# Optimization experiments

Hardware: AMD Instinct MI355X
Metric: run time of the kernel (lower is better)

## Reference

```python
import jax, jax.numpy as jnp
import numpy as np

LAYERS = 30
LAYERS_PER_STACK = 10  # layers // stacks
UPSAMPLE_SCALES = (10, 8)


def _c1x1(w, x):
    # 1x1 conv: w [O,C], x [B,C,T] -> [B,O,T]
    return jnp.einsum('oc,bct->bot', w, x)


def setup_inputs() -> dict:
    key = jax.random.key(0)
    ks = jax.random.split(key, 16)
    B, T, F = 4, 32000, 400
    s = 0.1  # weight scale to keep gates unsaturated
    inp = {
        'x': jax.random.normal(ks[0], (B, 256, T), jnp.float32),
        'c': jax.random.normal(ks[1], (B, 80, F), jnp.float32),
        'first_w': jax.random.normal(ks[2], (64, 256), jnp.float32) * s,
        'first_b': jnp.zeros((64,), jnp.float32),
        'conv_w': jax.random.normal(ks[3], (LAYERS, 128, 64, 2), jnp.float32) * s,
        'conv_b': jnp.zeros((LAYERS, 128), jnp.float32),
        'cond_w': jax.random.normal(ks[4], (LAYERS, 128, 80), jnp.float32) * s,
        'out_w': jax.random.normal(ks[5], (LAYERS, 64, 64), jnp.float32) * s,
        'out_b': jnp.zeros((LAYERS, 64), jnp.float32),
        'skip_w': jax.random.normal(ks[6], (LAYERS, 64, 64), jnp.float32) * s,
        'skip_b': jnp.zeros((LAYERS, 64), jnp.float32),
        'last1_w': jax.random.normal(ks[7], (64, 64), jnp.float32) * s,
        'last1_b': jnp.zeros((64,), jnp.float32),
        'last2_w': jax.random.normal(ks[8], (256, 64), jnp.float32) * s,
        'last2_b': jnp.zeros((256,), jnp.float32),
        'conv_in_w': jax.random.normal(ks[9], (80, 80), jnp.float32) * s,
        # upsample smoothing kernels, torch init: constant 1/kernel_size
        'up_w0': jnp.full((2 * 10 + 1,), 1.0 / (2 * 10 + 1), jnp.float32),
        'up_w1': jnp.full((2 * 8 + 1,), 1.0 / (2 * 8 + 1), jnp.float32),
    }
    return inp


def _wavenet(x, c, first_w, first_b, conv_w, conv_b, cond_w, out_w, out_b,
             skip_w, skip_b, last1_w, last1_b, last2_w, last2_b, conv_in_w,
             up_w0, up_w1):
    # --- ConvInUpsampleNetwork (aux_context_window=0 -> conv_in is 1x1, no bias) ---
    c = _c1x1(conv_in_w, c)  # [B,80,F]
    C = c.shape[1]
    for scale, w in zip(UPSAMPLE_SCALES, (up_w0, up_w1)):
        c = jnp.repeat(c, scale, axis=2)  # nearest interpolate along time
        rhs = jnp.broadcast_to(w[None, None, :], (C, 1, w.shape[0]))  # depthwise avg
        c = jax.lax.conv_general_dilated(
            c, rhs, window_strides=(1,), padding=[(scale, scale)],
            feature_group_count=C, dimension_numbers=('NCH', 'OIH', 'NCH'))
    # c now [B,80,T] with T = F*80 matching x
    T = x.shape[2]

    # --- first 1x1 conv ---
    h = _c1x1(first_w, x) + first_b[None, :, None]  # [B,64,T]

    skips = jnp.zeros_like(h[:, :64, :]) * 0.0  # [B,64,T]
    skips = 0.0
    for l in range(LAYERS):
        d = 2 ** (l % LAYERS_PER_STACK)  # dilation; padding = (k-1)*d = d
        xp = jnp.pad(h, ((0, 0), (0, 0), (d, 0)))  # causal left pad
        # dilated conv, kernel_size=2: taps at t-d and t
        g = (jnp.einsum('oc,bct->bot', conv_w[l, :, :, 0], xp[:, :, :T])
             + jnp.einsum('oc,bct->bot', conv_w[l, :, :, 1], xp[:, :, d:d + T])
             + conv_b[l][None, :, None])  # [B,128,T]
        g = g + _c1x1(cond_w[l], c)  # conditioning (split(a,b)+split(ca,cb) == split(g+cc))
        a, b = jnp.split(g, 2, axis=1)
        z = jnp.tanh(a) * jax.nn.sigmoid(b)  # [B,64,T]
        skips = skips + _c1x1(skip_w[l], z) + skip_b[l][None, :, None]
        h = h + _c1x1(out_w[l], z) + out_b[l][None, :, None]

    # --- last conv layers: ReLU, 1x1, ReLU, 1x1 ---
    o = jax.nn.relu(skips)
    o = _c1x1(last1_w, o) + last1_b[None, :, None]
    o = jax.nn.relu(o)
    o = _c1x1(last2_w, o) + last2_b[None, :, None]
    return o  # [B,256,T]


def reference(x, c, first_w, first_b, conv_w, conv_b, cond_w, out_w, out_b,
              skip_w, skip_b, last1_w, last1_b, last2_w, last2_b, conv_in_w,
              up_w0, up_w1):
    return _wavenet(x, c, first_w, first_b, conv_w, conv_b, cond_w, out_w,
                    out_b, skip_w, skip_b, last1_w, last1_b, last2_w, last2_b,
                    conv_in_w, up_w0, up_w1)
```

## Files before the change

kernel.cpp:

```cpp
#include <hip/hip_runtime.h>
#include <math.h>

#define T_TOTAL 32000
#define BATCH 4
#define TT 64
#define TTL 32
#define TTF 32

typedef __bf16 bf16x8 __attribute__((ext_vector_type(8)));
typedef float f32x4 __attribute__((ext_vector_type(4)));
typedef unsigned int uint4v __attribute__((ext_vector_type(4)));
typedef unsigned int uint2v __attribute__((ext_vector_type(2)));

__device__ __forceinline__ unsigned short f2b(float f) {
    unsigned int u = __float_as_uint(f);
    u += 0x7FFFu + ((u >> 16) & 1u);
    return (unsigned short)(u >> 16);
}
__device__ __forceinline__ unsigned int f2b2(float lo, float hi) {
    return (unsigned int)f2b(lo) | ((unsigned int)f2b(hi) << 16);
}
__device__ __forceinline__ bf16x8 ld_bf8(const unsigned short* p) {
    return __builtin_bit_cast(bf16x8, *(const uint4v*)p);
}
__device__ __forceinline__ float fast_sigmoid(float x) {
    return __builtin_amdgcn_rcpf(1.0f + __expf(-x));
}
__device__ __forceinline__ float fast_tanh(float x) {
    return 1.0f - 2.0f * __builtin_amdgcn_rcpf(1.0f + __expf(2.0f * x));
}

__global__ void k_pack(const float* __restrict__ conv_w, const float* __restrict__ cond_w,
                       const float* __restrict__ skip_w, const float* __restrict__ out_w,
                       const float* __restrict__ first_w, const float* __restrict__ last1_w,
                       const float* __restrict__ last2_w,
                       unsigned short* __restrict__ wgp, unsigned short* __restrict__ wzp,
                       unsigned short* __restrict__ fwp, unsigned short* __restrict__ l1p,
                       unsigned short* __restrict__ l2p) {
    int i = blockIdx.x * blockDim.x + threadIdx.x;
    if (i < 860160) {
        int l = i / 28672, r = i % 28672;
        int o = r / 224, k = r % 224;
        float v;
        if (k < 64)       v = conv_w[(((size_t)l * 128 + o) * 64 + k) * 2 + 0];
        else if (k < 128) v = conv_w[(((size_t)l * 128 + o) * 64 + (k - 64)) * 2 + 1];
        else if (k < 208) v = cond_w[((size_t)l * 128 + o) * 80 + (k - 128)];
        else              v = 0.0f;
        wgp[i] = f2b(v);
        return;
    }
    i -= 860160;
    if (i < 245760) {
        int l = i / 8192, rr = (i % 8192) / 64, k = i % 64;
        float v = (rr < 64) ? skip_w[((size_t)l * 64 + rr) * 64 + k]
                            : out_w[((size_t)l * 64 + (rr - 64)) * 64 + k];
        wzp[i] = f2b(v);
        return;
    }
    i -= 245760;
    if (i < 16384) { fwp[i] = f2b(first_w[i]); return; }
    i -= 16384;
    if (i < 4096) { l1p[i] = f2b(last1_w[i]); return; }
    i -= 4096;
    if (i < 16384) { l2p[i] = f2b(last2_w[i]); return; }
}

__global__ void k_convin(const float* __restrict__ c, const float* __restrict__ w,
                         float* __restrict__ c1) {
    int idx = blockIdx.x * blockDim.x + threadIdx.x;
    if (idx >= BATCH * 80 * 400) return;
    int f = idx % 400;
    int o = (idx / 400) % 80;
    int b = idx / (400 * 80);
    const float* cb = c + (size_t)b * 80 * 400 + f;
    const float* wr = w + o * 80;
    float acc = 0.f;
    #pragma unroll 8
    for (int j = 0; j < 80; ++j) acc += wr[j] * cb[(size_t)j * 400];
    c1[idx] = acc;
}

__global__ void k_up0(const float* __restrict__ c1, const float* __restrict__ w,
                      float* __restrict__ c2) {
    int idx = blockIdx.x * blockDim.x + threadIdx.x;
    if (idx >= BATCH * 80 * 4000) return;
    int t = idx % 4000;
    int ch = idx / 4000;
    int u = t / 10, r = t - u * 10;
    float w0 = 0.f, w1 = 0.f, w2 = 0.f;
    #pragma unroll
    for (int j = 0; j < 21; ++j) {
        float wj = w[j];
        int a = r - 10 + j;
        if (a < 0) w0 += wj;
        else if (a < 10) w1 += wj;
        else w2 += wj;
    }
    const float* src = c1 + (size_t)ch * 400;
    float s0 = (u >= 1) ? src[u - 1] : 0.f;
    float s1 = src[u];
    float s2 = (u + 1 < 400) ? src[u + 1] : 0.f;
    c2[idx] = w0 * s0 + w1 * s1 + w2 * s2;
}

__global__ __launch_bounds__(256) void k_up1b(const float* __restrict__ c2,
                                              const float* __restrict__ w,
                                              unsigned short* __restrict__ cupb) {
    __shared__ float S[80][13];
    __shared__ float W[8][4];
    const int b = blockIdx.y, t0 = blockIdx.x * 64;
    const int tid = threadIdx.x;
    const int u0 = t0 >> 3;

    for (int i = tid; i < 800; i += 256) {
        int ch = i / 10, uu = i % 10;
        int u = u0 - 1 + uu;
        float v = 0.f;
        if (u >= 0 && u < 4000) v = c2[((size_t)b * 80 + ch) * 4000 + u];
        S[ch][uu] = v;
    }
    if (tid < 24) {
        int r = tid / 3, k = tid % 3;
        int jlo = (k == 0) ? 0 : (k == 1 ? 8 - r : 16 - r);
        int jhi = (k == 0) ? 7 - r : (k == 1 ? 15 - r : 16);
        float a = 0.f;
        for (int j = jlo; j <= jhi; ++j) a += w[j];
        W[r][k] = a;
    }
    __syncthreads();

    unsigned short* ob = cupb + ((size_t)b * T_TOTAL + t0) * 96;
    for (int i = tid; i < 64 * 96; i += 256) {
        int ch = i % 96;
        int tl = i / 96;
        float acc = 0.f;
        if (ch < 80) {
            int r = tl & 7, ub = tl >> 3;
            acc = W[r][0] * S[ch][ub] + W[r][1] * S[ch][ub + 1] + W[r][2] * S[ch][ub + 2];
        }
        ob[i] = f2b(acc);
    }
}

#define XFS 266
__global__ __launch_bounds__(256, 8) void k_first(
    const float* __restrict__ x, const unsigned short* __restrict__ fwp,
    const float* __restrict__ fb, float* __restrict__ h0) {
    __shared__ unsigned short Xf[TTF * XFS];
    const int b = blockIdx.y, t0 = blockIdx.x * TTF, tid = threadIdx.x;
    const int lane = tid & 63;
    const int wv = __builtin_amdgcn_readfirstlane(tid >> 6);
    const int l15 = lane & 15, q = lane >> 4;

    for (int i = tid; i < 2048; i += 256) {
        int ch = i >> 3;
        int t4 = (i & 7) << 2;
        const float* xr = x + ((size_t)b * 256 + ch) * T_TOTAL + t0 + t4;
        float4 u = *(const float4*)xr;
        int base = t4 * XFS + ch;
        Xf[base + 0 * XFS] = f2b(u.x);
        Xf[base + 1 * XFS] = f2b(u.y);
        Xf[base + 2 * XFS] = f2b(u.z);
        Xf[base + 3 * XFS] = f2b(u.w);
    }
    __syncthreads();

    f32x4 acc[2] = {};
    const unsigned short* wr = fwp + (size_t)(16 * wv + l15) * 256;
    #pragma unroll
    for (int ks = 0; ks < 8; ++ks) {
        bf16x8 aA = ld_bf8(wr + ks * 32 + q * 8);
        #pragma unroll
        for (int tt = 0; tt < 2; ++tt) {
            bf16x8 bb = ld_bf8(&Xf[(tt * 16 + l15) * XFS + ks * 32 + q * 8]);
            acc[tt] = __builtin_amdgcn_mfma_f32_16x16x32_bf16(aA, bb, acc[tt], 0, 0, 0);
        }
    }
    const float4 fbv = *(const float4*)&fb[16 * wv + 4 * q];
    float* hob = h0 + (size_t)b * T_TOTAL * 64;
    #pragma unroll
    for (int tt = 0; tt < 2; ++tt) {
        size_t base = (size_t)(t0 + tt * 16 + l15) * 64 + 16 * wv + 4 * q;
        float4 ho;
        ho.x = acc[tt][0] + fbv.x;
        ho.y = acc[tt][1] + fbv.y;
        ho.z = acc[tt][2] + fbv.z;
        ho.w = acc[tt][3] + fbv.w;
        *(float4*)(hob + base) = ho;
    }
}

__global__ __launch_bounds__(256, 8) void k_layer(
    const float* __restrict__ h_in, float* __restrict__ h_out,
    float* __restrict__ skips, const unsigned short* __restrict__ cupb,
    const unsigned short* __restrict__ wgp_l, const unsigned short* __restrict__ wzp_l,
    const float* __restrict__ cb_l, const float* __restrict__ ob_l,
    const float* __restrict__ sb_l, int d, int first) {
    __shared__ unsigned short Xl[TTL * 224];
    __shared__ unsigned short zs[TTL * 72];
    const int b = blockIdx.y, t0 = blockIdx.x * TTL, tid = threadIdx.x;
    const int lane = tid & 63;
    const int wv = __builtin_amdgcn_readfirstlane(tid >> 6);
    const int l15 = lane & 15, q = lane >> 4;

    const float* hb = h_in + (size_t)b * T_TOTAL * 64;
    {
        int i = tid;
        int t = i >> 3, cb8 = (i & 7) << 3;
        const float4* p1 = (const float4*)(hb + (size_t)(t0 + t) * 64 + cb8);
        float4 u0 = p1[0], u1 = p1[1];
        uint4v v1;
        v1.x = f2b2(u0.x, u0.y); v1.y = f2b2(u0.z, u0.w);
        v1.z = f2b2(u1.x, u1.y); v1.w = f2b2(u1.z, u1.w);
        *(uint4v*)&Xl[t * 224 + 64 + cb8] = v1;
        int td = t0 + t - d;
        uint4v v0 = {0u, 0u, 0u, 0u};
        if (td >= 0) {
            const float4* p0 = (const float4*)(hb + (size_t)td * 64 + cb8);
            float4 w0 = p0[0], w1 = p0[1];
            v0.x = f2b2(w0.x, w0.y); v0.y = f2b2(w0.z, w0.w);
            v0.z = f2b2(w1.x, w1.y); v0.w = f2b2(w1.z, w1.w);
        }
        *(uint4v*)&Xl[t * 224 + cb8] = v0;
    }
    const unsigned short* cbb = cupb + (size_t)b * T_TOTAL * 96;
    for (int i = tid; i < 384; i += 256) {
        int t = i / 12, j = (i % 12) << 3;
        *(uint4v*)&Xl[t * 224 + 128 + j] = *(const uint4v*)&cbb[(size_t)(t0 + t) * 96 + j];
    }
    __syncthreads();

    f32x4 accA[2] = {}, accG[2] = {};
    const unsigned short* wrow_a = wgp_l + (size_t)(16 * wv + l15) * 224;
    const unsigned short* wrow_g = wgp_l + (size_t)(64 + 16 * wv + l15) * 224;
    #pragma unroll
    for (int ks = 0; ks < 7; ++ks) {
        bf16x8 aA = ld_bf8(wrow_a + ks * 32 + q * 8);
        bf16x8 aG = ld_bf8(wrow_g + ks * 32 + q * 8);
        #pragma unroll
        for (int tt = 0; tt < 2; ++tt) {
            bf16x8 bb = ld_bf8(&Xl[(tt * 16 + l15) * 224 + ks * 32 + q * 8]);
            accA[tt] = __builtin_amdgcn_mfma_f32_16x16x32_bf16(aA, bb, accA[tt], 0, 0, 0);
            accG[tt] = __builtin_amdgcn_mfma_f32_16x16x32_bf16(aG, bb, accG[tt], 0, 0, 0);
        }
    }
    const float4 cbA = *(const float4*)&cb_l[16 * wv + 4 * q];
    const float4 cbG = *(const float4*)&cb_l[64 + 16 * wv + 4 * q];
    #pragma unroll
    for (int tt = 0; tt < 2; ++tt) {
        int t = tt * 16 + l15;
        float z0 = fast_tanh(accA[tt][0] + cbA.x) * fast_sigmoid(accG[tt][0] + cbG.x);
        float z1 = fast_tanh(accA[tt][1] + cbA.y) * fast_sigmoid(accG[tt][1] + cbG.y);
        float z2 = fast_tanh(accA[tt][2] + cbA.z) * fast_sigmoid(accG[tt][2] + cbG.z);
        float z3 = fast_tanh(accA[tt][3] + cbA.w) * fast_sigmoid(accG[tt][3] + cbG.w);
        uint2v zv;
        zv.x = f2b2(z0, z1);
        zv.y = f2b2(z2, z3);
        *(uint2v*)&zs[t * 72 + 16 * wv + 4 * q] = zv;
    }
    __syncthreads();

    f32x4 accS[2] = {}, accO[2] = {};
    const unsigned short* zrow_s = wzp_l + (size_t)(16 * wv + l15) * 64;
    const unsigned short* zrow_o = wzp_l + (size_t)(64 + 16 * wv + l15) * 64;
    #pragma unroll
    for (int ks = 0; ks < 2; ++ks) {
        bf16x8 aS = ld_bf8(zrow_s + ks * 32 + q * 8);
        bf16x8 aO = ld_bf8(zrow_o + ks * 32 + q * 8);
        #pragma unroll
        for (int tt = 0; tt < 2; ++tt) {
            bf16x8 bb = ld_bf8(&zs[(tt * 16 + l15) * 72 + ks * 32 + q * 8]);
            accS[tt] = __builtin_amdgcn_mfma_f32_16x16x32_bf16(aS, bb, accS[tt], 0, 0, 0);
            accO[tt] = __builtin_amdgcn_mfma_f32_16x16x32_bf16(aO, bb, accO[tt], 0, 0, 0);
        }
    }
    const float4 sbv = *(const float4*)&sb_l[16 * wv + 4 * q];
    const float4 obv = *(const float4*)&ob_l[16 * wv + 4 * q];
    float* hob = h_out + (size_t)b * T_TOTAL * 64;
    float* skb = skips + (size_t)b * T_TOTAL * 64;
    #pragma unroll
    for (int tt = 0; tt < 2; ++tt) {
        size_t base = (size_t)(t0 + tt * 16 + l15) * 64 + 16 * wv + 4 * q;
        float4 hi = *(const float4*)(hb + base);
        float4 ho;
        ho.x = hi.x + accO[tt][0] + obv.x;
        ho.y = hi.y + accO[tt][1] + obv.y;
        ho.z = hi.z + accO[tt][2] + obv.z;
        ho.w = hi.w + accO[tt][3] + obv.w;
        *(float4*)(hob + base) = ho;
        float4 sv;
        if (first) {
            sv.x = accS[tt][0] + sbv.x;
            sv.y = accS[tt][1] + sbv.y;
            sv.z = accS[tt][2] + sbv.z;
            sv.w = accS[tt][3] + sbv.w;
        } else {
            float4 sp = *(const float4*)(skb + base);
            sv.x = sp.x + accS[tt][0] + sbv.x;
            sv.y = sp.y + accS[tt][1] + sbv.y;
            sv.z = sp.z + accS[tt][2] + sbv.z;
            sv.w = sp.w + accS[tt][3] + sbv.w;
        }
        *(float4*)(skb + base) = sv;
    }
}

__global__ __launch_bounds__(256) void k_last(
    const float* __restrict__ skips, const unsigned short* __restrict__ l1p,
    const float* __restrict__ b1, const unsigned short* __restrict__ l2p,
    const float* __restrict__ b2, float* __restrict__ out) {
    __shared__ unsigned short sp[64 * 72];
    __shared__ unsigned short o2s[64 * 72];
    const int b = blockIdx.y, t0 = blockIdx.x * TT, tid = threadIdx.x;
    const int lane = tid & 63;
    const int wv = __builtin_amdgcn_readfirstlane(tid >> 6);
    const int l15 = lane & 15, q = lane >> 4;

    const float* skb = skips + (size_t)b * T_TOTAL * 64;
    for (int i = tid; i < 512; i += 256) {
        int t = i >> 3, cb8 = (i & 7) << 3;
        const float4* p = (const float4*)(skb + (size_t)(t0 + t) * 64 + cb8);
        float4 u0 = p[0], u1 = p[1];
        uint4v v;
        v.x = f2b2(fmaxf(u0.x, 0.f), fmaxf(u0.y, 0.f));
        v.y = f2b2(fmaxf(u0.z, 0.f), fmaxf(u0.w, 0.f));
        v.z = f2b2(fmaxf(u1.x, 0.f), fmaxf(u1.y, 0.f));
        v.w = f2b2(fmaxf(u1.z, 0.f), fmaxf(u1.w, 0.f));
        *(uint4v*)&sp[t * 72 + cb8] = v;
    }
    __syncthreads();

    f32x4 a1[4] = {};
    const unsigned short* w1r = l1p + (size_t)(16 * wv + l15) * 64;
    #pragma unroll
    for (int ks = 0; ks < 2; ++ks) {
        bf16x8 aA = ld_bf8(w1r + ks * 32 + q * 8);
        #pragma unroll
        for (int tt = 0; tt < 4; ++tt) {
            bf16x8 bb = ld_bf8(&sp[(tt * 16 + l15) * 72 + ks * 32 + q * 8]);
            a1[tt] = __builtin_amdgcn_mfma_f32_16x16x32_bf16(aA, bb, a1[tt], 0, 0, 0);
        }
    }
    const float4 b1v = *(const float4*)&b1[16 * wv + 4 * q];
    #pragma unroll
    for (int tt = 0; tt < 4; ++tt) {
        int t = tt * 16 + l15;
        float z0 = fmaxf(a1[tt][0] + b1v.x, 0.f);
        float z1 = fmaxf(a1[tt][1] + b1v.y, 0.f);
        float z2 = fmaxf(a1[tt][2] + b1v.z, 0.f);
        float z3 = fmaxf(a1[tt][3] + b1v.w, 0.f);
        uint2v zv;
        zv.x = f2b2(z0, z1);
        zv.y = f2b2(z2, z3);
        *(uint2v*)&o2s[t * 72 + 16 * wv + 4 * q] = zv;
    }
    __syncthreads();

    f32x4 a2[4][4] = {};
    #pragma unroll
    for (int ks = 0; ks < 2; ++ks) {
        bf16x8 aw[4];
        #pragma unroll
        for (int j = 0; j < 4; ++j)
            aw[j] = ld_bf8(l2p + (size_t)(64 * wv + 16 * j + l15) * 64 + ks * 32 + q * 8);
        #pragma unroll
        for (int tt = 0; tt < 4; ++tt) {
            bf16x8 bb = ld_bf8(&o2s[(tt * 16 + l15) * 72 + ks * 32 + q * 8]);
            #pragma unroll
            for (int j = 0; j < 4; ++j)
                a2[j][tt] = __builtin_amdgcn_mfma_f32_16x16x32_bf16(aw[j], bb, a2[j][tt], 0, 0, 0);
        }
    }
    float* ob = out + (size_t)b * 256 * T_TOTAL;
    #pragma unroll
    for (int j = 0; j < 4; ++j) {
        int o0 = 64 * wv + 16 * j + 4 * q;
        float4 b2v = *(const float4*)&b2[o0];
        #pragma unroll
        for (int tt = 0; tt < 4; ++tt) {
            int t = t0 + tt * 16 + l15;
            ob[(size_t)(o0 + 0) * T_TOTAL + t] = a2[j][tt][0] + b2v.x;
            ob[(size_t)(o0 + 1) * T_TOTAL + t] = a2[j][tt][1] + b2v.y;
            ob[(size_t)(o0 + 2) * T_TOTAL + t] = a2[j][tt][2] + b2v.z;
            ob[(size_t)(o0 + 3) * T_TOTAL + t] = a2[j][tt][3] + b2v.w;
        }
    }
}

extern "C" void kernel_launch(void* const* d_in, const int* in_sizes, int n_in,
                              void* d_out, int out_size, void* d_ws, size_t ws_size,
                              hipStream_t stream) {
    const float* x         = (const float*)d_in[0];
    const float* c         = (const float*)d_in[1];
    const float* first_w   = (const float*)d_in[2];
    const float* first_b   = (const float*)d_in[3];
    const float* conv_w    = (const float*)d_in[4];
    const float* conv_b    = (const float*)d_in[5];
    const float* cond_w    = (const float*)d_in[6];
    const float* out_w     = (const float*)d_in[7];
    const float* out_b     = (const float*)d_in[8];
    const float* skip_w    = (const float*)d_in[9];
    const float* skip_b    = (const float*)d_in[10];
    const float* last1_w   = (const float*)d_in[11];
    const float* last1_b   = (const float*)d_in[12];
    const float* last2_w   = (const float*)d_in[13];
    const float* last2_b   = (const float*)d_in[14];
    const float* conv_in_w = (const float*)d_in[15];
    const float* up_w0     = (const float*)d_in[16];
    const float* up_w1     = (const float*)d_in[17];

    unsigned char* base = (unsigned char*)d_ws;
    float* c1            = (float*)(base + 0);
    float* c2            = (float*)(base + 512000);
    unsigned short* cupb = (unsigned short*)(base + 5632000);
    float* hA            = (float*)(base + 30208000);
    float* hB            = (float*)(base + 62976000);
    float* skips         = (float*)(base + 95744000);
    unsigned short* wgp  = (unsigned short*)(base + 128512000);
    unsigned short* wzp  = (unsigned short*)(base + 130232320);
    unsigned short* fwp  = (unsigned short*)(base + 130723840);
    unsigned short* l1p  = (unsigned short*)(base + 130756608);
    unsigned short* l2p  = (unsigned short*)(base + 130764800);

    k_pack<<<(1142784 + 255) / 256, 256, 0, stream>>>(
        conv_w, cond_w, skip_w, out_w, first_w, last1_w, last2_w,
        wgp, wzp, fwp, l1p, l2p);
    k_convin<<<(BATCH * 80 * 400 + 255) / 256, 256, 0, stream>>>(c, conv_in_w, c1);
    k_up0<<<(BATCH * 80 * 4000 + 255) / 256, 256, 0, stream>>>(c1, up_w0, c2);
    dim3 upg(T_TOTAL / 64, BATCH);
    k_up1b<<<upg, 256, 0, stream>>>(c2, up_w1, cupb);

    dim3 gridF(T_TOTAL / TTF, BATCH);
    k_first<<<gridF, 256, 0, stream>>>(x, fwp, first_b, hA);

    dim3 gridL(T_TOTAL / TTL, BATCH);
    float* hin = hA;
    float* hout = hB;
    for (int l = 0; l < 30; ++l) {
        int d = 1 << (l % 10);
        k_layer<<<gridL, 256, 0, stream>>>(
            hin, hout, skips, cupb,
            wgp + (size_t)l * 128 * 224, wzp + (size_t)l * 128 * 64,
            conv_b + (size_t)l * 128, out_b + (size_t)l * 64, skip_b + (size_t)l * 64,
            d, l == 0 ? 1 : 0);
        float* tmp = hin; hin = hout; hout = tmp;
    }

    dim3 grid(T_TOTAL / TT, BATCH);
    k_last<<<grid, 256, 0, stream>>>(skips, l1p, last1_b, l2p, last2_b, (float*)d_out);
}
```

Baseline: 1.659 ms.

## Fuse pairs of small-dilation WaveNet layers into one kernel with halo recompute

Adds k_layer2, which computes two consecutive residual layers (dilations 1/2, 4/8, 16/32) in one launch. It loads a 32-sample halo and recomputes the first layer's output over that halo in shared memory, so the intermediate h never makes a round trip through global memory and skips is read-modify-written once per pair. The remaining layers use k_layer with the time tile widened from 32 to 64 and padded LDS strides. In exchange, the fused kernel does about 50% extra first-layer work, uses more registers and LDS, and runs at lower occupancy (launch bounds 2 and 4).

```diff
diff --git a/kernel.cpp b/kernel.cpp
--- a/kernel.cpp
+++ b/kernel.cpp
@@ -4,8 +4,9 @@
 #define T_TOTAL 32000
 #define BATCH 4
 #define TT 64
-#define TTL 32
 #define TTF 32
+#define X1S 232
+#define X2S 136
 
 typedef __bf16 bf16x8 __attribute__((ext_vector_type(8)));
 typedef float f32x4 __attribute__((ext_vector_type(4)));
@@ -29,6 +30,7 @@
 __device__ __forceinline__ float fast_tanh(float x) {
     return 1.0f - 2.0f * __builtin_amdgcn_rcpf(1.0f + __expf(2.0f * x));
 }
+#define MFMA(a, b, c) __builtin_amdgcn_mfma_f32_16x16x32_bf16((a), (b), (c), 0, 0, 0)
 
 __global__ void k_pack(const float* __restrict__ conv_w, const float* __restrict__ cond_w,
                        const float* __restrict__ skip_w, const float* __restrict__ out_w,
@@ -173,7 +175,7 @@
         #pragma unroll
         for (int tt = 0; tt < 2; ++tt) {
             bf16x8 bb = ld_bf8(&Xf[(tt * 16 + l15) * XFS + ks * 32 + q * 8]);
-            acc[tt] = __builtin_amdgcn_mfma_f32_16x16x32_bf16(aA, bb, acc[tt], 0, 0, 0);
+            acc[tt] = MFMA(aA, bb, acc[tt]);
         }
     }
     const float4 fbv = *(const float4*)&fb[16 * wv + 4 * q];
@@ -190,29 +192,28 @@
     }
 }
 
-__global__ __launch_bounds__(256, 8) void k_layer(
+__global__ __launch_bounds__(256, 4) void k_layer(
     const float* __restrict__ h_in, float* __restrict__ h_out,
     float* __restrict__ skips, const unsigned short* __restrict__ cupb,
     const unsigned short* __restrict__ wgp_l, const unsigned short* __restrict__ wzp_l,
     const float* __restrict__ cb_l, const float* __restrict__ ob_l,
     const float* __restrict__ sb_l, int d, int first) {
-    __shared__ unsigned short Xl[TTL * 224];
-    __shared__ unsigned short zs[TTL * 72];
-    const int b = blockIdx.y, t0 = blockIdx.x * TTL, tid = threadIdx.x;
+    __shared__ __attribute__((aligned(16))) unsigned short Xl[TT * X1S];
+    __shared__ __attribute__((aligned(16))) unsigned short zs[TT * 72];
+    const int b = blockIdx.y, t0 = blockIdx.x * TT, tid = threadIdx.x;
     const int lane = tid & 63;
     const int wv = __builtin_amdgcn_readfirstlane(tid >> 6);
     const int l15 = lane & 15, q = lane >> 4;
 
     const float* hb = h_in + (size_t)b * T_TOTAL * 64;
-    {
-        int i = tid;
+    for (int i = tid; i < 512; i += 256) {
         int t = i >> 3, cb8 = (i & 7) << 3;
         const float4* p1 = (const float4*)(hb + (size_t)(t0 + t) * 64 + cb8);
         float4 u0 = p1[0], u1 = p1[1];
         uint4v v1;
         v1.x = f2b2(u0.x, u0.y); v1.y = f2b2(u0.z, u0.w);
         v1.z = f2b2(u1.x, u1.y); v1.w = f2b2(u1.z, u1.w);
-        *(uint4v*)&Xl[t * 224 + 64 + cb8] = v1;
+        *(uint4v*)&Xl[t * X1S + 64 + cb8] = v1;
         int td = t0 + t - d;
         uint4v v0 = {0u, 0u, 0u, 0u};
         if (td >= 0) {
@@ -221,16 +222,16 @@
             v0.x = f2b2(w0.x, w0.y); v0.y = f2b2(w0.z, w0.w);
             v0.z = f2b2(w1.x, w1.y); v0.w = f2b2(w1.z, w1.w);
         }
-        *(uint4v*)&Xl[t * 224 + cb8] = v0;
+        *(uint4v*)&Xl[t * X1S + cb8] = v0;
     }
     const unsigned short* cbb = cupb + (size_t)b * T_TOTAL * 96;
-    for (int i = tid; i < 384; i += 256) {
+    for (int i = tid; i < 768; i += 256) {
         int t = i / 12, j = (i % 12) << 3;
-        *(uint4v*)&Xl[t * 224 + 128 + j] = *(const uint4v*)&cbb[(size_t)(t0 + t) * 96 + j];
-    }
-    __syncthreads();
-
-    f32x4 accA[2] = {}, accG[2] = {};
+        *(uint4v*)&Xl[t * X1S + 128 + j] = *(const uint4v*)&cbb[(size_t)(t0 + t) * 96 + j];
+    }
+    __syncthreads();
+
+    f32x4 accA[4] = {}, accG[4] = {};
     const unsigned short* wrow_a = wgp_l + (size_t)(16 * wv + l15) * 224;
     const unsigned short* wrow_g = wgp_l + (size_t)(64 + 16 * wv + l15) * 224;
     #pragma unroll
@@ -238,16 +239,16 @@
         bf16x8 aA = ld_bf8(wrow_a + ks * 32 + q * 8);
         bf16x8 aG = ld_bf8(wrow_g + ks * 32 + q * 8);
         #pragma unroll
-        for (int tt = 0; tt < 2; ++tt) {
-            bf16x8 bb = ld_bf8(&Xl[(tt * 16 + l15) * 224 + ks * 32 + q * 8]);
-            accA[tt] = __builtin_amdgcn_mfma_f32_16x16x32_bf16(aA, bb, accA[tt], 0, 0, 0);
-            accG[tt] = __builtin_amdgcn_mfma_f32_16x16x32_bf16(aG, bb, accG[tt], 0, 0, 0);
+        for (int tt = 0; tt < 4; ++tt) {
+            bf16x8 bb = ld_bf8(&Xl[(tt * 16 + l15) * X1S + ks * 32 + q * 8]);
+            accA[tt] = MFMA(aA, bb, accA[tt]);
+            accG[tt] = MFMA(aG, bb, accG[tt]);
         }
     }
     const float4 cbA = *(const float4*)&cb_l[16 * wv + 4 * q];
     const float4 cbG = *(const float4*)&cb_l[64 + 16 * wv + 4 * q];
     #pragma unroll
-    for (int tt = 0; tt < 2; ++tt) {
+    for (int tt = 0; tt < 4; ++tt) {
         int t = tt * 16 + l15;
         float z0 = fast_tanh(accA[tt][0] + cbA.x) * fast_sigmoid(accG[tt][0] + cbG.x);
         float z1 = fast_tanh(accA[tt][1] + cbA.y) * fast_sigmoid(accG[tt][1] + cbG.y);
@@ -260,7 +261,7 @@
     }
     __syncthreads();
 
-    f32x4 accS[2] = {}, accO[2] = {};
+    f32x4 accS[4] = {}, accO[4] = {};
     const unsigned short* zrow_s = wzp_l + (size_t)(16 * wv + l15) * 64;
     const unsigned short* zrow_o = wzp_l + (size_t)(64 + 16 * wv + l15) * 64;
     #pragma unroll
@@ -268,10 +269,10 @@
         bf16x8 aS = ld_bf8(zrow_s + ks * 32 + q * 8);
         bf16x8 aO = ld_bf8(zrow_o + ks * 32 + q * 8);
         #pragma unroll
-        for (int tt = 0; tt < 2; ++tt) {
+        for (int tt = 0; tt < 4; ++tt) {
             bf16x8 bb = ld_bf8(&zs[(tt * 16 + l15) * 72 + ks * 32 + q * 8]);
-            accS[tt] = __builtin_amdgcn_mfma_f32_16x16x32_bf16(aS, bb, accS[tt], 0, 0, 0);
-            accO[tt] = __builtin_amdgcn_mfma_f32_16x16x32_bf16(aO, bb, accO[tt], 0, 0, 0);
+            accS[tt] = MFMA(aS, bb, accS[tt]);
+            accO[tt] = MFMA(aO, bb, accO[tt]);
         }
     }
     const float4 sbv = *(const float4*)&sb_l[16 * wv + 4 * q];
@@ -279,7 +280,7 @@
     float* hob = h_out + (size_t)b * T_TOTAL * 64;
     float* skb = skips + (size_t)b * T_TOTAL * 64;
     #pragma unroll
-    for (int tt = 0; tt < 2; ++tt) {
+    for (int tt = 0; tt < 4; ++tt) {
         size_t base = (size_t)(t0 + tt * 16 + l15) * 64 + 16 * wv + 4 * q;
         float4 hi = *(const float4*)(hb + base);
         float4 ho;
@@ -305,12 +306,243 @@
     }
 }
 
+__global__ __launch_bounds__(256, 2) void k_layer2(
+    const float* __restrict__ h_in, float* __restrict__ h_out,
+    float* __restrict__ skips, const unsigned short* __restrict__ cupb,
+    const unsigned short* __restrict__ wg1, const unsigned short* __restrict__ wg2,
+    const unsigned short* __restrict__ wz1, const unsigned short* __restrict__ wz2,
+    const float* __restrict__ cb1, const float* __restrict__ cb2,
+    const float* __restrict__ ob1, const float* __restrict__ ob2,
+    const float* __restrict__ sb1, const float* __restrict__ sb2,
+    int d1, int d2, int first) {
+    __shared__ __attribute__((aligned(16))) unsigned short X1[96 * X1S];
+    __shared__ __attribute__((aligned(16))) unsigned short ZS[96 * 72];
+    __shared__ __attribute__((aligned(16))) unsigned short X2[64 * X2S];
+    const int b = blockIdx.y, t0 = blockIdx.x * 64, ts = t0 - 32;
+    const int tid = threadIdx.x;
+    const int lane = tid & 63;
+    const int wv = __builtin_amdgcn_readfirstlane(tid >> 6);
+    const int l15 = lane & 15, q = lane >> 4;
+    const int chb = 16 * wv + 4 * q;
+    const int chunk = 4 * wv + q;
+
+    const float* hb = h_in + (size_t)b * T_TOTAL * 64;
+    for (int i = tid; i < 768; i += 256) {
+        int r = i >> 3, cb8 = (i & 7) << 3;
+        int t = ts + r;
+        uint4v v1 = {0u, 0u, 0u, 0u}, v0 = {0u, 0u, 0u, 0u};
+        if (t >= 0) {
+            const float4* p1 = (const float4*)(hb + (size_t)t * 64 + cb8);
+            float4 u0 = p1[0], u1 = p1[1];
+            v1.x = f2b2(u0.x, u0.y); v1.y = f2b2(u0.z, u0.w);
+            v1.z = f2b2(u1.x, u1.y); v1.w = f2b2(u1.z, u1.w);
+        }
+        int td = ts + r - d1;
+        if (td >= 0) {
+            const float4* p0 = (const float4*)(hb + (size_t)td * 64 + cb8);
+            float4 w0 = p0[0], w1 = p0[1];
+            v0.x = f2b2(w0.x, w0.y); v0.y = f2b2(w0.z, w0.w);
+            v0.z = f2b2(w1.x, w1.y); v0.w = f2b2(w1.z, w1.w);
+        }
+        *(uint4v*)&X1[r * X1S + 64 + cb8] = v1;
+        *(uint4v*)&X1[r * X1S + cb8] = v0;
+    }
+    const unsigned short* cbb = cupb + (size_t)b * T_TOTAL * 96;
+    for (int i = tid; i < 1152; i += 256) {
+        int r = i / 12, j = (i % 12) << 3;
+        int t = ts + r;
+        uint4v cv = {0u, 0u, 0u, 0u};
+        if (t >= 0) cv = *(const uint4v*)&cbb[(size_t)t * 96 + j];
+        *(uint4v*)&X1[r * X1S + 128 + j] = cv;
+    }
+    __syncthreads();
+
+    f32x4 A1[6] = {}, G1[6] = {};
+    {
+        const unsigned short* wra = wg1 + (size_t)(16 * wv + l15) * 224;
+        const unsigned short* wrg = wg1 + (size_t)(64 + 16 * wv + l15) * 224;
+        #pragma unroll
+        for (int ks = 0; ks < 7; ++ks) {
+            bf16x8 aA = ld_bf8(wra + ks * 32 + q * 8);
+            bf16x8 aG = ld_bf8(wrg + ks * 32 + q * 8);
+            #pragma unroll
+            for (int tt = 0; tt < 6; ++tt) {
+                bf16x8 bb = ld_bf8(&X1[(tt * 16 + l15) * X1S + ks * 32 + q * 8]);
+                A1[tt] = MFMA(aA, bb, A1[tt]);
+                G1[tt] = MFMA(aG, bb, G1[tt]);
+            }
+        }
+    }
+    {
+        const float4 cA = *(const float4*)&cb1[chb];
+        const float4 cG = *(const float4*)&cb1[64 + chb];
+        #pragma unroll
+        for (int tt = 0; tt < 6; ++tt) {
+            int r = tt * 16 + l15;
+            float z0 = fast_tanh(A1[tt][0] + cA.x) * fast_sigmoid(G1[tt][0] + cG.x);
+            float z1 = fast_tanh(A1[tt][1] + cA.y) * fast_sigmoid(G1[tt][1] + cG.y);
+            float z2 = fast_tanh(A1[tt][2] + cA.z) * fast_sigmoid(G1[tt][2] + cG.z);
+            float z3 = fast_tanh(A1[tt][3] + cA.w) * fast_sigmoid(G1[tt][3] + cG.w);
+            uint2v zv;
+            zv.x = f2b2(z0, z1);
+            zv.y = f2b2(z2, z3);
+            *(uint2v*)&ZS[r * 72 + chb] = zv;
+        }
+    }
+    __syncthreads();
+
+    f32x4 O1[6] = {}, S1[4] = {};
+    {
+        const unsigned short* zrs = wz1 + (size_t)(16 * wv + l15) * 64;
+        const unsigned short* zro = wz1 + (size_t)(64 + 16 * wv + l15) * 64;
+        #pragma unroll
+        for (int ks = 0; ks < 2; ++ks) {
+            bf16x8 aS = ld_bf8(zrs + ks * 32 + q * 8);
+            bf16x8 aO = ld_bf8(zro + ks * 32 + q * 8);
+            #pragma unroll
+            for (int tt = 0; tt < 6; ++tt) {
+                bf16x8 bb = ld_bf8(&ZS[(tt * 16 + l15) * 72 + ks * 32 + q * 8]);
+                O1[tt] = MFMA(aO, bb, O1[tt]);
+                if (tt >= 2) S1[tt - 2] = MFMA(aS, bb, S1[tt - 2]);
+            }
+        }
+    }
+    {
+        const float4 ov = *(const float4*)&ob1[chb];
+        #pragma unroll
+        for (int tt = 0; tt < 6; ++tt) {
+            int r = tt * 16 + l15;
+            int t = ts + r;
+            float4 hl = make_float4(0.f, 0.f, 0.f, 0.f);
+            if (t >= 0) {
+                float4 hi = *(const float4*)(hb + (size_t)t * 64 + chb);
+                hl.x = hi.x + O1[tt][0] + ov.x;
+                hl.y = hi.y + O1[tt][1] + ov.y;
+                hl.z = hi.z + O1[tt][2] + ov.z;
+                hl.w = hi.w + O1[tt][3] + ov.w;
+            }
+            uint2v hbv;
+            hbv.x = f2b2(hl.x, hl.y);
+            hbv.y = f2b2(hl.z, hl.w);
+            if (r >= 32) {
+                int swz = chunk ^ (r & 15);
+                *(float4*)&X1[r * X1S + 8 * swz] = hl;
+                *(uint2v*)&X2[(r - 32) * X2S + 64 + chb] = hbv;
+            }
+            int rr = r - 32 + d2;
+            if (rr >= 0 && rr < 64) *(uint2v*)&X2[rr * X2S + chb] = hbv;
+        }
+    }
+    __syncthreads();
+
+    f32x4 A2[4] = {}, G2[4] = {};
+    {
+        const unsigned short* wra = wg2 + (size_t)(16 * wv + l15) * 224;
+        const unsigned short* wrg = wg2 + (size_t)(64 + 16 * wv + l15) * 224;
+        #pragma unroll
+        for (int ks = 0; ks < 4; ++ks) {
+            bf16x8 aA = ld_bf8(wra + ks * 32 + q * 8);
+            bf16x8 aG = ld_bf8(wrg + ks * 32 + q * 8);
+            #pragma unroll
+            for (int tt = 0; tt < 4; ++tt) {
+                bf16x8 bb = ld_bf8(&X2[(tt * 16 + l15) * X2S + ks * 32 + q * 8]);
+                A2[tt] = MFMA(aA, bb, A2[tt]);
+                G2[tt] = MFMA(aG, bb, G2[tt]);
+            }
+        }
+        #pragma unroll
+        for (int ks = 4; ks < 7; ++ks) {
+            bf16x8 aA = ld_bf8(wra + ks * 32 + q * 8);
+            bf16x8 aG = ld_bf8(wrg + ks * 32 + q * 8);
+            #pragma unroll
+            for (int tt = 0; tt < 4; ++tt) {
+                bf16x8 bb = ld_bf8(&X1[(tt * 16 + l15 + 32) * X1S + 128 + (ks - 4) * 32 + q * 8]);
+                A2[tt] = MFMA(aA, bb, A2[tt]);
+                G2[tt] = MFMA(aG, bb, G2[tt]);
+            }
+        }
+    }
+    {
+        const float4 cA = *(const float4*)&cb2[chb];
+        const float4 cG = *(const float4*)&cb2[64 + chb];
+        #pragma unroll
+        for (int tt = 0; tt < 4; ++tt) {
+            int r = tt * 16 + l15;
+            float z0 = fast_tanh(A2[tt][0] + cA.x) * fast_sigmoid(G2[tt][0] + cG.x);
+            float z1 = fast_tanh(A2[tt][1] + cA.y) * fast_sigmoid(G2[tt][1] + cG.y);
+            float z2 = fast_tanh(A2[tt][2] + cA.z) * fast_sigmoid(G2[tt][2] + cG.z);
+            float z3 = fast_tanh(A2[tt][3] + cA.w) * fast_sigmoid(G2[tt][3] + cG.w);
+            uint2v zv;
+            zv.x = f2b2(z0, z1);
+            zv.y = f2b2(z2, z3);
+            *(uint2v*)&ZS[r * 72 + chb] = zv;
+        }
+    }
+    __syncthreads();
+
+    f32x4 O2[4] = {}, S2[4] = {};
+    {
+        const unsigned short* zrs = wz2 + (size_t)(16 * wv + l15) * 64;
+        const unsigned short* zro = wz2 + (size_t)(64 + 16 * wv + l15) * 64;
+        #pragma unroll
+        for (int ks = 0; ks < 2; ++ks) {
+            bf16x8 aS = ld_bf8(zrs + ks * 32 + q * 8);
+            bf16x8 aO = ld_bf8(zro + ks * 32 + q * 8);
+            #pragma unroll
+            for (int tt = 0; tt < 4; ++tt) {
+                bf16x8 bb = ld_bf8(&ZS[(tt * 16 + l15) * 72 + ks * 32 + q * 8]);
+                S2[tt] = MFMA(aS, bb, S2[tt]);
+                O2[tt] = MFMA(aO, bb, O2[tt]);
+            }
+        }
+    }
+    {
+        const float4 o2v = *(const float4*)&ob2[chb];
+        const float4 s1v = *(const float4*)&sb1[chb];
+        const float4 s2v = *(const float4*)&sb2[chb];
+        float* hob = h_out + (size_t)b * T_TOTAL * 64;
+        float* skb = skips + (size_t)b * T_TOTAL * 64;
+        #pragma unroll
+        for (int tt = 0; tt < 4; ++tt) {
+            int r = 32 + tt * 16 + l15;
+            int t = t0 + tt * 16 + l15;
+            int swz = chunk ^ (r & 15);
+            float4 hl = *(const float4*)&X1[r * X1S + 8 * swz];
+            size_t base = (size_t)t * 64 + chb;
+            float4 ho;
+            ho.x = hl.x + O2[tt][0] + o2v.x;
+            ho.y = hl.y + O2[tt][1] + o2v.y;
+            ho.z = hl.z + O2[tt][2] + o2v.z;
+            ho.w = hl.w + O2[tt][3] + o2v.w;
+            *(float4*)(hob + base) = ho;
+            float4 sv;
+            if (first) {
+                sv.x = S1[tt][0] + s1v.x;
+                sv.y = S1[tt][1] + s1v.y;
+                sv.z = S1[tt][2] + s1v.z;
+                sv.w = S1[tt][3] + s1v.w;
+            } else {
+                float4 sp = *(const float4*)(skb + base);
+                sv.x = sp.x + S1[tt][0] + s1v.x;
+                sv.y = sp.y + S1[tt][1] + s1v.y;
+                sv.z = sp.z + S1[tt][2] + s1v.z;
+                sv.w = sp.w + S1[tt][3] + s1v.w;
+            }
+            sv.x = sv.x + S2[tt][0] + s2v.x;
+            sv.y = sv.y + S2[tt][1] + s2v.y;
+            sv.z = sv.z + S2[tt][2] + s2v.z;
+            sv.w = sv.w + S2[tt][3] + s2v.w;
+            *(float4*)(skb + base) = sv;
+        }
+    }
+}
+
 __global__ __launch_bounds__(256) void k_last(
     const float* __restrict__ skips, const unsigned short* __restrict__ l1p,
     const float* __restrict__ b1, const unsigned short* __restrict__ l2p,
     const float* __restrict__ b2, float* __restrict__ out) {
-    __shared__ unsigned short sp[64 * 72];
-    __shared__ unsigned short o2s[64 * 72];
+    __shared__ __attribute__((aligned(16))) unsigned short sp[64 * 72];
+    __shared__ __attribute__((aligned(16))) unsigned short o2s[64 * 72];
     const int b = blockIdx.y, t0 = blockIdx.x * TT, tid = threadIdx.x;
     const int lane = tid & 63;
     const int wv = __builtin_amdgcn_readfirstlane(tid >> 6);
@@ -338,7 +570,7 @@
         #pragma unroll
         for (int tt = 0; tt < 4; ++tt) {
             bf16x8 bb = ld_bf8(&sp[(tt * 16 + l15) * 72 + ks * 32 + q * 8]);
-            a1[tt] = __builtin_amdgcn_mfma_f32_16x16x32_bf16(aA, bb, a1[tt], 0, 0, 0);
+            a1[tt] = MFMA(aA, bb, a1[tt]);
         }
     }
     const float4 b1v = *(const float4*)&b1[16 * wv + 4 * q];
@@ -368,7 +600,7 @@
             bf16x8 bb = ld_bf8(&o2s[(tt * 16 + l15) * 72 + ks * 32 + q * 8]);
             #pragma unroll
             for (int j = 0; j < 4; ++j)
-                a2[j][tt] = __builtin_amdgcn_mfma_f32_16x16x32_bf16(aw[j], bb, a2[j][tt], 0, 0, 0);
+                a2[j][tt] = MFMA(aw[j], bb, a2[j][tt]);
         }
     }
     float* ob = out + (size_t)b * 256 * T_TOTAL;
@@ -433,19 +665,34 @@
     dim3 gridF(T_TOTAL / TTF, BATCH);
     k_first<<<gridF, 256, 0, stream>>>(x, fwp, first_b, hA);
 
-    dim3 gridL(T_TOTAL / TTL, BATCH);
+    dim3 grid(T_TOTAL / TT, BATCH);
     float* hin = hA;
     float* hout = hB;
-    for (int l = 0; l < 30; ++l) {
-        int d = 1 << (l % 10);
-        k_layer<<<gridL, 256, 0, stream>>>(
-            hin, hout, skips, cupb,
-            wgp + (size_t)l * 128 * 224, wzp + (size_t)l * 128 * 64,
-            conv_b + (size_t)l * 128, out_b + (size_t)l * 64, skip_b + (size_t)l * 64,
-            d, l == 0 ? 1 : 0);
-        float* tmp = hin; hin = hout; hout = tmp;
-    }
-
-    dim3 grid(T_TOTAL / TT, BATCH);
+    for (int s = 0; s < 3; ++s) {
+        for (int p = 0; p < 3; ++p) {
+            int l = s * 10 + 2 * p;
+            int d1 = 1 << (2 * p);
+            k_layer2<<<grid, 256, 0, stream>>>(
+                hin, hout, skips, cupb,
+                wgp + (size_t)l * 28672, wgp + (size_t)(l + 1) * 28672,
+                wzp + (size_t)l * 8192, wzp + (size_t)(l + 1) * 8192,
+                conv_b + (size_t)l * 128, conv_b + (size_t)(l + 1) * 128,
+                out_b + (size_t)l * 64, out_b + (size_t)(l + 1) * 64,
+                skip_b + (size_t)l * 64, skip_b + (size_t)(l + 1) * 64,
+                d1, 2 * d1, (l == 0) ? 1 : 0);
+            float* tmp = hin; hin = hout; hout = tmp;
+        }
+        for (int j = 6; j < 10; ++j) {
+            int l = s * 10 + j;
+            int d = 1 << j;
+            k_layer<<<grid, 256, 0, stream>>>(
+                hin, hout, skips, cupb,
+                wgp + (size_t)l * 28672, wzp + (size_t)l * 8192,
+                conv_b + (size_t)l * 128, out_b + (size_t)l * 64,
+                skip_b + (size_t)l * 64, d, 0);
+            float* tmp = hin; hin = hout; hout = tmp;
+        }
+    }
+
     k_last<<<grid, 256, 0, stream>>>(skips, l1p, last1_b, l2p, last2_b, (float*)d_out);
 }
```

After: 1.441 ms. 1.15x faster.
